# Optimization experiments

Hardware: AMD Instinct MI355X
Metric: run time of the kernel (lower is better)

The kernel has to match this reference:

```python
import jax, jax.numpy as jnp
import numpy as np

N, C_TOTAL, C, H, W = 8, 448, 100, 56, 56


def setup_inputs() -> dict:
    key = jax.random.key(0)
    k1, k2, k3, k4 = jax.random.split(key, 4)
    fmaps = jax.random.normal(k1, (N, C_TOTAL, H, W), dtype=jnp.float32)
    select_index = jax.random.randint(k2, (C,), 0, C_TOTAL)
    mean = jax.random.normal(k3, (C, H, W), dtype=jnp.float32)
    # Per-pixel inverse covariance must be PSD so the quadratic form is >= 0
    A = jax.random.normal(k4, (C, C, H, W), dtype=jnp.float32)
    cov = jnp.einsum('cehw,dehw->cdhw', A, A) / jnp.float32(C)  # (C,C,H,W), PSD per pixel
    return {
        'fmaps': fmaps,
        'select_index': select_index,
        'mean': mean,
        'cov': cov,
        'min_score': jnp.float32(0.0),
        'max_score': jnp.float32(50.0),
    }


def reference(fmaps, select_index, mean, cov, min_score, max_score):
    # x_ = fmaps[:, select_index, ...] - mean  -> (N, C, H, W)
    x = fmaps[:, select_index, :, :] - mean[None]
    # left = sum_c x[n,c,h,w] * cov[c,d,h,w]  (per-pixel matvec), avoids (N,C,C,H,W) intermediate
    left = jnp.einsum('nchw,cdhw->ndhw', x, cov)
    # per-pixel Mahalanobis distance
    s_map = jnp.sqrt(jnp.sum(x * left, axis=1))  # (N, H, W)
    # bilinear upsample x4 (torch Upsample align_corners=False == half-pixel linear resize)
    score_map = jax.image.resize(s_map, (s_map.shape[0], 4 * H, 4 * W), method='linear')
    scores = (score_map - min_score) / (max_score - min_score)
    return jnp.squeeze(scores)
```

## Files before the change

kernel.cpp:

```cpp
#include <hip/hip_runtime.h>
#include <math.h>

#define NN 8
#define C_TOTAL 448
#define CC 100
#define HH 56
#define WW 56
#define HW (HH*WW)
#define NPIX4 (HW/4)
#define OH 224
#define OW 224
#define NT4 13
#define NG 25

typedef __attribute__((ext_vector_type(4))) _Float16 half4;
typedef __attribute__((ext_vector_type(8))) _Float16 half8;
typedef __attribute__((ext_vector_type(4))) float    f32x4;

__device__ __forceinline__ f32x4 cvtlo(const half8 h) {
    return __builtin_convertvector(__builtin_shufflevector(h, h, 0, 1, 2, 3), f32x4);
}
__device__ __forceinline__ f32x4 cvthi(const half8 h) {
    return __builtin_convertvector(__builtin_shufflevector(h, h, 4, 5, 6, 7), f32x4);
}
__device__ __forceinline__ f32x4 fmav(const f32x4 a, const f32x4 b, const f32x4 c) {
    f32x4 r;
    r.x = fmaf(a.x, b.x, c.x);
    r.y = fmaf(a.y, b.y, c.y);
    r.z = fmaf(a.z, b.z, c.z);
    r.w = fmaf(a.w, b.w, c.w);
    return r;
}

__global__ __launch_bounds__(256) void prep_x_kernel(
    const float* __restrict__ fmaps, const int* __restrict__ sel,
    const float* __restrict__ mean, half4* __restrict__ xbuf,
    float* __restrict__ smap)
{
    const int idx = blockIdx.x * 256 + threadIdx.x;
    if (idx < NN * NPIX4) {
        ((float4*)smap)[idx] = make_float4(0.f, 0.f, 0.f, 0.f);
    }
    if (idx >= CC * NPIX4) return;
    const int quad = idx % NPIX4;
    const int c    = idx / NPIX4;

    const float4* f4 = (const float4*)fmaps;
    const float4  m  = ((const float4*)mean)[(size_t)c * NPIX4 + quad];
    const int     sc = sel[c];

    half4 hv[NN];
#pragma unroll
    for (int n = 0; n < NN; ++n) {
        const float4 f = f4[((size_t)n * C_TOTAL + sc) * NPIX4 + quad];
        half4 h;
        h.x = (_Float16)(f.x - m.x);
        h.y = (_Float16)(f.y - m.y);
        h.z = (_Float16)(f.z - m.z);
        h.w = (_Float16)(f.w - m.w);
        hv[n] = h;
    }
    half4* dst = xbuf + ((size_t)c * NPIX4 + quad) * NN;
#pragma unroll
    for (int n = 0; n < NN; ++n) dst[n] = hv[n];
}

__global__ __launch_bounds__(512, 3) void qform_kernel(
    const half4* __restrict__ xbuf, const float* __restrict__ cov,
    float* __restrict__ smap)
{
    __shared__ f32x4 lred[8 * 4 * 64];

    const int tile = blockIdx.x % NT4;
    const int k    = blockIdx.x / NT4;
    const int a    = 4 * k;

    const int w    = threadIdx.x >> 6;
    const int dph  = w & 3;
    const int imgh = w >> 2;
    const int lane = threadIdx.x & 63;
    const int qraw = tile * 64 + lane;
    const bool valid = qraw < NPIX4;
    const int quad = valid ? qraw : (NPIX4 - 1);

    const f32x4* c4 = (const f32x4*)cov;

    f32x4 acc[4][4];
#pragma unroll
    for (int i = 0; i < 4; ++i)
#pragma unroll
        for (int j = 0; j < 4; ++j) acc[i][j] = (f32x4){0.f, 0.f, 0.f, 0.f};

    {
        const int d0 = a + dph;
        const half8* xp = (const half8*)(xbuf + ((size_t)d0 * NPIX4 + quad) * NN + imgh * 4);
        const half8 hA = xp[0];
        const half8 hB = xp[1];
        f32x4 xv[4];
        xv[0] = cvtlo(hA); xv[1] = cvthi(hA);
        xv[2] = cvtlo(hB); xv[3] = cvthi(hB);
#pragma unroll
        for (int i = 0; i < 4; ++i) {
            if (i <= dph) {
                f32x4 cv = __builtin_nontemporal_load(
                    &c4[((size_t)(a + i) * CC + d0) * NPIX4 + quad]);
                if (i == dph) cv *= 0.5f;
#pragma unroll
                for (int j = 0; j < 4; ++j) acc[i][j] = fmav(xv[j], cv, acc[i][j]);
            }
        }
    }

    for (int d = a + 4 + dph; d < CC; d += 4) {
        const half8* xp = (const half8*)(xbuf + ((size_t)d * NPIX4 + quad) * NN + imgh * 4);
        const half8 hA = xp[0];
        const half8 hB = xp[1];
        f32x4 xv[4];
        xv[0] = cvtlo(hA); xv[1] = cvthi(hA);
        xv[2] = cvtlo(hB); xv[3] = cvthi(hB);

        const size_t base = ((size_t)a * CC + d) * NPIX4 + quad;
#pragma unroll
        for (int i = 0; i < 4; ++i) {
            const f32x4 cv = __builtin_nontemporal_load(&c4[base + (size_t)i * CC * NPIX4]);
#pragma unroll
            for (int j = 0; j < 4; ++j) acc[i][j] = fmav(xv[j], cv, acc[i][j]);
        }
    }

    {
        f32x4 part[4];
#pragma unroll
        for (int j = 0; j < 4; ++j) part[j] = (f32x4){0.f, 0.f, 0.f, 0.f};
#pragma unroll
        for (int i = 0; i < 4; ++i) {
            const half8* xp = (const half8*)(xbuf + ((size_t)(a + i) * NPIX4 + quad) * NN + imgh * 4);
            const half8 hA = xp[0];
            const half8 hB = xp[1];
            part[0] = fmav(cvtlo(hA), acc[i][0], part[0]);
            part[1] = fmav(cvthi(hA), acc[i][1], part[1]);
            part[2] = fmav(cvtlo(hB), acc[i][2], part[2]);
            part[3] = fmav(cvthi(hB), acc[i][3], part[3]);
        }
#pragma unroll
        for (int j = 0; j < 4; ++j) {
            part[j] = part[j] + part[j];
            lred[(w * 4 + j) * 64 + lane] = part[j];
        }
    }
    __syncthreads();

    {
        const int im = w;
        const int ih = im >> 2;
        const int sl = im & 3;
        f32x4 s = (f32x4){0.f, 0.f, 0.f, 0.f};
#pragma unroll
        for (int dp = 0; dp < 4; ++dp) {
            s = s + lred[((ih * 4 + dp) * 4 + sl) * 64 + lane];
        }
        if (valid) {
            float* dst = smap + (size_t)im * HW + (size_t)qraw * 4;
            atomicAdd(dst + 0, s.x);
            atomicAdd(dst + 1, s.y);
            atomicAdd(dst + 2, s.z);
            atomicAdd(dst + 3, s.w);
        }
    }
}

__global__ __launch_bounds__(256) void upsample_kernel(
    const float* __restrict__ smap,
    const float* __restrict__ minp, const float* __restrict__ maxp,
    float* __restrict__ out)
{
    const int idx = blockIdx.x * 256 + threadIdx.x;
    const int total = NN * OH * OW;
    if (idx >= total) return;

    const int ox = idx % OW;
    const int oy = (idx / OW) % OH;
    const int n  = idx / (OW * OH);

    const float fy = oy * 0.25f - 0.375f;
    const float fx = ox * 0.25f - 0.375f;

    int y0 = (int)floorf(fy);
    int x0 = (int)floorf(fx);
    const float wy = fy - (float)y0;
    const float wx = fx - (float)x0;
    int y1 = min(y0 + 1, HH - 1); y0 = max(y0, 0);
    int x1 = min(x0 + 1, WW - 1); x0 = max(x0, 0);

    const float* s = smap + (size_t)n * HW;
    const float v00 = sqrtf(fmaxf(s[y0 * WW + x0], 0.f));
    const float v01 = sqrtf(fmaxf(s[y0 * WW + x1], 0.f));
    const float v10 = sqrtf(fmaxf(s[y1 * WW + x0], 0.f));
    const float v11 = sqrtf(fmaxf(s[y1 * WW + x1], 0.f));

    const float v = (1.0f - wy) * ((1.0f - wx) * v00 + wx * v01)
                  +          wy * ((1.0f - wx) * v10 + wx * v11);

    const float mn = *minp;
    const float mx = *maxp;
    out[idx] = (v - mn) / (mx - mn);
}

extern "C" void kernel_launch(void* const* d_in, const int* in_sizes, int n_in,
                              void* d_out, int out_size, void* d_ws, size_t ws_size,
                              hipStream_t stream)
{
    const float* fmaps = (const float*)d_in[0];
    const int*   sel   = (const int*)  d_in[1];
    const float* mean  = (const float*)d_in[2];
    const float* cov   = (const float*)d_in[3];
    const float* minp  = (const float*)d_in[4];
    const float* maxp  = (const float*)d_in[5];
    float* out = (float*)d_out;

    half4* xbuf = (half4*)d_ws;
    float* smap = (float*)((char*)d_ws + (size_t)CC*NPIX4*NN*8);

    {
        const int total = CC * NPIX4;
        prep_x_kernel<<<(total + 255) / 256, 256, 0, stream>>>(fmaps, sel, mean, xbuf, smap);
    }
    qform_kernel<<<NG * NT4, 512, 0, stream>>>(xbuf, cov, smap);
    {
        const int total = NN * OH * OW;
        upsample_kernel<<<(total + 255) / 256, 256, 0, stream>>>(smap, minp, maxp, out);
    }
}
```

Baseline: 221.8 us.

## Split long triangular row groups across two blocks and rebalance warp work

The quadratic-form kernel previously gave each block one 4-row group of the upper triangle, so the early groups carried far more columns than the late ones and the grid was small and unbalanced. Now the first twelve row groups are split at their column midpoint into two blocks each, growing the grid from 325 to 481 blocks. Within a block each warp now owns two rows and handles alternate columns, with the column loop unrolled by two, and the occupancy hint rises to 4 blocks per CU. This is meant to even out per-block work and improve latency hiding, at the cost of more atomics and more repeated x loads.

```diff
diff --git a/kernel.cpp b/kernel.cpp
--- a/kernel.cpp
+++ b/kernel.cpp
@@ -12,6 +12,8 @@
 #define OW 224
 #define NT4 13
 #define NG 25
+#define KSPLIT 12
+#define NKIND (2*KSPLIT + (NG - KSPLIT))
 
 typedef __attribute__((ext_vector_type(4))) _Float16 half4;
 typedef __attribute__((ext_vector_type(8))) _Float16 half8;
@@ -65,83 +67,136 @@
     for (int n = 0; n < NN; ++n) dst[n] = hv[n];
 }
 
-__global__ __launch_bounds__(512, 3) void qform_kernel(
+__global__ __launch_bounds__(512, 4) void qform_kernel(
     const half4* __restrict__ xbuf, const float* __restrict__ cov,
     float* __restrict__ smap)
 {
     __shared__ f32x4 lred[8 * 4 * 64];
 
     const int tile = blockIdx.x % NT4;
-    const int k    = blockIdx.x / NT4;
-    const int a    = 4 * k;
+    const int kind = blockIdx.x / NT4;
+    int k, h, split;
+    if (kind < 2 * KSPLIT) { k = kind >> 1; h = kind & 1; split = 1; }
+    else                   { k = kind - KSPLIT; h = 0; split = 0; }
+    const int a   = 4 * k;
+    const int L   = CC - a;
+    const int mid = a + ((L + 1) >> 1);
 
     const int w    = threadIdx.x >> 6;
-    const int dph  = w & 3;
+    const int dph  = w & 1;
+    const int rh   = (w >> 1) & 1;
     const int imgh = w >> 2;
     const int lane = threadIdx.x & 63;
     const int qraw = tile * 64 + lane;
     const bool valid = qraw < NPIX4;
     const int quad = valid ? qraw : (NPIX4 - 1);
 
-    const f32x4* c4 = (const f32x4*)cov;
-
-    f32x4 acc[4][4];
-#pragma unroll
-    for (int i = 0; i < 4; ++i)
+    const int r0 = a + 2 * rh;
+    const int r1 = r0 + 1;
+
+    const f32x4* c4  = (const f32x4*)cov;
+    const half8* xb8 = (const half8*)xbuf;
+
+    f32x4 acc[2][4];
+#pragma unroll
+    for (int i = 0; i < 2; ++i)
 #pragma unroll
         for (int j = 0; j < 4; ++j) acc[i][j] = (f32x4){0.f, 0.f, 0.f, 0.f};
 
-    {
-        const int d0 = a + dph;
-        const half8* xp = (const half8*)(xbuf + ((size_t)d0 * NPIX4 + quad) * NN + imgh * 4);
+    int lo, hi;
+    if (split && h == 1) {
+        lo = mid + (((mid ^ (a + dph)) & 1));
+        hi = CC;
+    } else {
+        hi = split ? mid : CC;
+        const int d0 = r0 + dph;
+        {
+            const half8* xp = xb8 + ((size_t)d0 * NPIX4 + quad) * 4 + imgh * 2;
+            const half8 hA = xp[0];
+            const half8 hB = xp[1];
+            f32x4 xv[4];
+            xv[0] = cvtlo(hA); xv[1] = cvthi(hA);
+            xv[2] = cvtlo(hB); xv[3] = cvthi(hB);
+            f32x4 cv0 = __builtin_nontemporal_load(&c4[((size_t)r0 * CC + d0) * NPIX4 + quad]);
+            if (dph == 0) {
+                cv0 *= 0.5f;
+#pragma unroll
+                for (int j = 0; j < 4; ++j) acc[0][j] = fmav(xv[j], cv0, acc[0][j]);
+            } else {
+#pragma unroll
+                for (int j = 0; j < 4; ++j) acc[0][j] = fmav(xv[j], cv0, acc[0][j]);
+                f32x4 cv1 = __builtin_nontemporal_load(&c4[((size_t)r1 * CC + d0) * NPIX4 + quad]);
+                cv1 *= 0.5f;
+#pragma unroll
+                for (int j = 0; j < 4; ++j) acc[1][j] = fmav(xv[j], cv1, acc[1][j]);
+            }
+        }
+        lo = r0 + dph + 2;
+    }
+
+    int d = lo;
+    for (; d + 2 < hi; d += 4) {
+        const half8* xp0 = xb8 + ((size_t)d * NPIX4 + quad) * 4 + imgh * 2;
+        const half8* xp1 = xb8 + ((size_t)(d + 2) * NPIX4 + quad) * 4 + imgh * 2;
+        const half8 a0 = xp0[0];
+        const half8 b0 = xp0[1];
+        const half8 a1 = xp1[0];
+        const half8 b1 = xp1[1];
+        const size_t cb0 = ((size_t)r0 * CC + d) * NPIX4 + quad;
+        const size_t cb1 = ((size_t)r1 * CC + d) * NPIX4 + quad;
+        const f32x4 c00 = __builtin_nontemporal_load(&c4[cb0]);
+        const f32x4 c10 = __builtin_nontemporal_load(&c4[cb1]);
+        const f32x4 c01 = __builtin_nontemporal_load(&c4[cb0 + 2 * NPIX4]);
+        const f32x4 c11 = __builtin_nontemporal_load(&c4[cb1 + 2 * NPIX4]);
+
+        {
+            f32x4 xv[4];
+            xv[0] = cvtlo(a0); xv[1] = cvthi(a0);
+            xv[2] = cvtlo(b0); xv[3] = cvthi(b0);
+#pragma unroll
+            for (int j = 0; j < 4; ++j) acc[0][j] = fmav(xv[j], c00, acc[0][j]);
+#pragma unroll
+            for (int j = 0; j < 4; ++j) acc[1][j] = fmav(xv[j], c10, acc[1][j]);
+        }
+        {
+            f32x4 xv[4];
+            xv[0] = cvtlo(a1); xv[1] = cvthi(a1);
+            xv[2] = cvtlo(b1); xv[3] = cvthi(b1);
+#pragma unroll
+            for (int j = 0; j < 4; ++j) acc[0][j] = fmav(xv[j], c01, acc[0][j]);
+#pragma unroll
+            for (int j = 0; j < 4; ++j) acc[1][j] = fmav(xv[j], c11, acc[1][j]);
+        }
+    }
+    if (d < hi) {
+        const half8* xp = xb8 + ((size_t)d * NPIX4 + quad) * 4 + imgh * 2;
         const half8 hA = xp[0];
         const half8 hB = xp[1];
+        const f32x4 c0 = __builtin_nontemporal_load(&c4[((size_t)r0 * CC + d) * NPIX4 + quad]);
+        const f32x4 c1 = __builtin_nontemporal_load(&c4[((size_t)r1 * CC + d) * NPIX4 + quad]);
         f32x4 xv[4];
         xv[0] = cvtlo(hA); xv[1] = cvthi(hA);
         xv[2] = cvtlo(hB); xv[3] = cvthi(hB);
 #pragma unroll
-        for (int i = 0; i < 4; ++i) {
-            if (i <= dph) {
-                f32x4 cv = __builtin_nontemporal_load(
-                    &c4[((size_t)(a + i) * CC + d0) * NPIX4 + quad]);
-                if (i == dph) cv *= 0.5f;
-#pragma unroll
-                for (int j = 0; j < 4; ++j) acc[i][j] = fmav(xv[j], cv, acc[i][j]);
-            }
-        }
-    }
-
-    for (int d = a + 4 + dph; d < CC; d += 4) {
-        const half8* xp = (const half8*)(xbuf + ((size_t)d * NPIX4 + quad) * NN + imgh * 4);
-        const half8 hA = xp[0];
-        const half8 hB = xp[1];
-        f32x4 xv[4];
-        xv[0] = cvtlo(hA); xv[1] = cvthi(hA);
-        xv[2] = cvtlo(hB); xv[3] = cvthi(hB);
-
-        const size_t base = ((size_t)a * CC + d) * NPIX4 + quad;
-#pragma unroll
-        for (int i = 0; i < 4; ++i) {
-            const f32x4 cv = __builtin_nontemporal_load(&c4[base + (size_t)i * CC * NPIX4]);
-#pragma unroll
-            for (int j = 0; j < 4; ++j) acc[i][j] = fmav(xv[j], cv, acc[i][j]);
-        }
-    }
-
-    {
+        for (int j = 0; j < 4; ++j) acc[0][j] = fmav(xv[j], c0, acc[0][j]);
+#pragma unroll
+        for (int j = 0; j < 4; ++j) acc[1][j] = fmav(xv[j], c1, acc[1][j]);
+    }
+
+    {
+        const half8* x0p = xb8 + ((size_t)r0 * NPIX4 + quad) * 4 + imgh * 2;
+        const half8* x1p = xb8 + ((size_t)r1 * NPIX4 + quad) * 4 + imgh * 2;
+        const half8 xa0 = x0p[0], xb0 = x0p[1];
+        const half8 xa1 = x1p[0], xb1 = x1p[1];
         f32x4 part[4];
-#pragma unroll
-        for (int j = 0; j < 4; ++j) part[j] = (f32x4){0.f, 0.f, 0.f, 0.f};
-#pragma unroll
-        for (int i = 0; i < 4; ++i) {
-            const half8* xp = (const half8*)(xbuf + ((size_t)(a + i) * NPIX4 + quad) * NN + imgh * 4);
-            const half8 hA = xp[0];
-            const half8 hB = xp[1];
-            part[0] = fmav(cvtlo(hA), acc[i][0], part[0]);
-            part[1] = fmav(cvthi(hA), acc[i][1], part[1]);
-            part[2] = fmav(cvtlo(hB), acc[i][2], part[2]);
-            part[3] = fmav(cvthi(hB), acc[i][3], part[3]);
-        }
+        part[0] = cvtlo(xa0) * acc[0][0];
+        part[1] = cvthi(xa0) * acc[0][1];
+        part[2] = cvtlo(xb0) * acc[0][2];
+        part[3] = cvthi(xb0) * acc[0][3];
+        part[0] = fmav(cvtlo(xa1), acc[1][0], part[0]);
+        part[1] = fmav(cvthi(xa1), acc[1][1], part[1]);
+        part[2] = fmav(cvtlo(xb1), acc[1][2], part[2]);
+        part[3] = fmav(cvthi(xb1), acc[1][3], part[3]);
 #pragma unroll
         for (int j = 0; j < 4; ++j) {
             part[j] = part[j] + part[j];
@@ -152,12 +207,12 @@
 
     {
         const int im = w;
-        const int ih = im >> 2;
+        const int sh = (im >> 2) * 4;
         const int sl = im & 3;
         f32x4 s = (f32x4){0.f, 0.f, 0.f, 0.f};
 #pragma unroll
-        for (int dp = 0; dp < 4; ++dp) {
-            s = s + lred[((ih * 4 + dp) * 4 + sl) * 64 + lane];
+        for (int sw = 0; sw < 4; ++sw) {
+            s = s + lred[((sh + sw) * 4 + sl) * 64 + lane];
         }
         if (valid) {
             float* dst = smap + (size_t)im * HW + (size_t)qraw * 4;
@@ -225,7 +280,7 @@
         const int total = CC * NPIX4;
         prep_x_kernel<<<(total + 255) / 256, 256, 0, stream>>>(fmaps, sel, mean, xbuf, smap);
     }
-    qform_kernel<<<NG * NT4, 512, 0, stream>>>(xbuf, cov, smap);
+    qform_kernel<<<NKIND * NT4, 512, 0, stream>>>(xbuf, cov, smap);
     {
         const int total = NN * OH * OW;
         upsample_kernel<<<(total + 255) / 256, 256, 0, stream>>>(smap, minp, maxp, out);
```

Measured after the change: 219.2 us. No clear change (-1.2%).

## Stage cov tiles into LDS with async global_load_lds double buffering

Applied to the files above, without the earlier changes.

The qform kernel now streams covariance rows into shared memory in chunks of 8 d-values using global_load_lds, double-buffered so the next chunk loads while the current one is consumed. Work across waves is re-split: each wave owns two of the four rows and alternates d parity, which halves the accumulator registers. Occupancy is raised from 3 to 4 blocks per CU. The cost is extra block-wide barriers per chunk and LDS traffic, and padded tail iterations are masked with zero weights.

```diff
diff --git a/kernel.cpp b/kernel.cpp
--- a/kernel.cpp
+++ b/kernel.cpp
@@ -12,6 +12,7 @@
 #define OW 224
 #define NT4 13
 #define NG 25
+#define CHB 8
 
 typedef __attribute__((ext_vector_type(4))) _Float16 half4;
 typedef __attribute__((ext_vector_type(8))) _Float16 half8;
@@ -31,6 +32,10 @@
     r.w = fmaf(a.w, b.w, c.w);
     return r;
 }
+
+#define GL_LDS(gp, lp) \
+  __builtin_amdgcn_global_load_lds((const __attribute__((address_space(1))) void*)(gp), \
+                                   (__attribute__((address_space(3))) void*)(lp), 16, 0, 0)
 
 __global__ __launch_bounds__(256) void prep_x_kernel(
     const float* __restrict__ fmaps, const int* __restrict__ sel,
@@ -65,83 +70,130 @@
     for (int n = 0; n < NN; ++n) dst[n] = hv[n];
 }
 
-__global__ __launch_bounds__(512, 3) void qform_kernel(
+__global__ __launch_bounds__(512, 4) void qform_kernel(
     const half4* __restrict__ xbuf, const float* __restrict__ cov,
     float* __restrict__ smap)
 {
-    __shared__ f32x4 lred[8 * 4 * 64];
+    __shared__ __align__(16) char ldsraw[2 * CHB * 4 * 64 * 16];
 
     const int tile = blockIdx.x % NT4;
     const int k    = blockIdx.x / NT4;
     const int a    = 4 * k;
 
     const int w    = threadIdx.x >> 6;
-    const int dph  = w & 3;
+    const int cph  = w & 1;
+    const int rh   = (w >> 1) & 1;
     const int imgh = w >> 2;
     const int lane = threadIdx.x & 63;
     const int qraw = tile * 64 + lane;
     const bool valid = qraw < NPIX4;
     const int quad = valid ? qraw : (NPIX4 - 1);
 
-    const f32x4* c4 = (const f32x4*)cov;
-
-    f32x4 acc[4][4];
-#pragma unroll
-    for (int i = 0; i < 4; ++i)
+    const int r0 = a + 2 * rh;
+    const int r1 = r0 + 1;
+
+    const half8* xb8 = (const half8*)xbuf;
+    f32x4* covlds = (f32x4*)ldsraw;
+
+    const int S0  = a + 4;
+    const int nch = (CC - S0 + CHB - 1) / CHB;
+
+    f32x4 acc[2][4];
+#pragma unroll
+    for (int i = 0; i < 2; ++i)
 #pragma unroll
         for (int j = 0; j < 4; ++j) acc[i][j] = (f32x4){0.f, 0.f, 0.f, 0.f};
 
-    {
-        const int d0 = a + dph;
-        const half8* xp = (const half8*)(xbuf + ((size_t)d0 * NPIX4 + quad) * NN + imgh * 4);
+    if (nch > 0) {
+        const int d  = S0 + w;
+        const int dc = (d < CC) ? d : (CC - 1);
+#pragma unroll
+        for (int i = 0; i < 4; ++i) {
+            const float* g = cov + ((size_t)(a + i) * CC + dc) * HW + (size_t)quad * 4;
+            GL_LDS(g, (char*)&covlds[((0 * CHB + w) * 4 + i) * 64]);
+        }
+    }
+
+#pragma unroll
+    for (int dd = 0; dd < 2; ++dd) {
+        const int d = a + 2 * dd + cph;
+        const half8* xp = xb8 + ((size_t)d * NPIX4 + quad) * 4 + imgh * 2;
         const half8 hA = xp[0];
         const half8 hB = xp[1];
         f32x4 xv[4];
         xv[0] = cvtlo(hA); xv[1] = cvthi(hA);
         xv[2] = cvtlo(hB); xv[3] = cvthi(hB);
 #pragma unroll
-        for (int i = 0; i < 4; ++i) {
-            if (i <= dph) {
+        for (int i = 0; i < 2; ++i) {
+            const int r = r0 + i;
+            if (r <= d) {
                 f32x4 cv = __builtin_nontemporal_load(
-                    &c4[((size_t)(a + i) * CC + d0) * NPIX4 + quad]);
-                if (i == dph) cv *= 0.5f;
+                    (const f32x4*)(cov + ((size_t)r * CC + d) * HW + (size_t)quad * 4));
+                if (r == d) cv *= 0.5f;
 #pragma unroll
                 for (int j = 0; j < 4; ++j) acc[i][j] = fmav(xv[j], cv, acc[i][j]);
             }
         }
     }
 
-    for (int d = a + 4 + dph; d < CC; d += 4) {
-        const half8* xp = (const half8*)(xbuf + ((size_t)d * NPIX4 + quad) * NN + imgh * 4);
-        const half8 hA = xp[0];
-        const half8 hB = xp[1];
-        f32x4 xv[4];
-        xv[0] = cvtlo(hA); xv[1] = cvthi(hA);
-        xv[2] = cvtlo(hB); xv[3] = cvthi(hB);
-
-        const size_t base = ((size_t)a * CC + d) * NPIX4 + quad;
-#pragma unroll
-        for (int i = 0; i < 4; ++i) {
-            const f32x4 cv = __builtin_nontemporal_load(&c4[base + (size_t)i * CC * NPIX4]);
-#pragma unroll
-            for (int j = 0; j < 4; ++j) acc[i][j] = fmav(xv[j], cv, acc[i][j]);
-        }
-    }
-
-    {
+    if (nch > 0) {
+        asm volatile("s_waitcnt vmcnt(0)" ::: "memory");
+        __syncthreads();
+        int buf = 0;
+        for (int ch = 0; ch < nch; ++ch) {
+            if (ch + 1 < nch) {
+                const int d  = S0 + (ch + 1) * CHB + w;
+                const int dc = (d < CC) ? d : (CC - 1);
+#pragma unroll
+                for (int i = 0; i < 4; ++i) {
+                    const float* g = cov + ((size_t)(a + i) * CC + dc) * HW + (size_t)quad * 4;
+                    GL_LDS(g, (char*)&covlds[(((buf ^ 1) * CHB + w) * 4 + i) * 64]);
+                }
+            }
+            const int cb = S0 + ch * CHB;
+#pragma unroll
+            for (int ci = 0; ci < 4; ++ci) {
+                const int cl = 2 * ci + cph;
+                const int d  = cb + cl;
+                const float wt = (d < CC) ? 1.f : 0.f;
+                const int  dc  = (d < CC) ? d : (CC - 1);
+                const half8* xp = xb8 + ((size_t)dc * NPIX4 + quad) * 4 + imgh * 2;
+                const half8 hA = xp[0];
+                const half8 hB = xp[1];
+                f32x4 xv[4];
+                xv[0] = cvtlo(hA); xv[1] = cvthi(hA);
+                xv[2] = cvtlo(hB); xv[3] = cvthi(hB);
+                f32x4 cv0 = covlds[((buf * CHB + cl) * 4 + 2 * rh + 0) * 64 + lane];
+                f32x4 cv1 = covlds[((buf * CHB + cl) * 4 + 2 * rh + 1) * 64 + lane];
+                cv0 *= wt;
+                cv1 *= wt;
+#pragma unroll
+                for (int j = 0; j < 4; ++j) acc[0][j] = fmav(xv[j], cv0, acc[0][j]);
+#pragma unroll
+                for (int j = 0; j < 4; ++j) acc[1][j] = fmav(xv[j], cv1, acc[1][j]);
+            }
+            asm volatile("s_waitcnt vmcnt(0)" ::: "memory");
+            __syncthreads();
+            buf ^= 1;
+        }
+    }
+
+    __syncthreads();
+    f32x4* lred = (f32x4*)ldsraw;
+    {
+        const half8* x0p = xb8 + ((size_t)r0 * NPIX4 + quad) * 4 + imgh * 2;
+        const half8* x1p = xb8 + ((size_t)r1 * NPIX4 + quad) * 4 + imgh * 2;
+        const half8 xa0 = x0p[0], xb0 = x0p[1];
+        const half8 xa1 = x1p[0], xb1 = x1p[1];
         f32x4 part[4];
-#pragma unroll
-        for (int j = 0; j < 4; ++j) part[j] = (f32x4){0.f, 0.f, 0.f, 0.f};
-#pragma unroll
-        for (int i = 0; i < 4; ++i) {
-            const half8* xp = (const half8*)(xbuf + ((size_t)(a + i) * NPIX4 + quad) * NN + imgh * 4);
-            const half8 hA = xp[0];
-            const half8 hB = xp[1];
-            part[0] = fmav(cvtlo(hA), acc[i][0], part[0]);
-            part[1] = fmav(cvthi(hA), acc[i][1], part[1]);
-            part[2] = fmav(cvtlo(hB), acc[i][2], part[2]);
-            part[3] = fmav(cvthi(hB), acc[i][3], part[3]);
-        }
+        part[0] = cvtlo(xa0) * acc[0][0];
+        part[1] = cvthi(xa0) * acc[0][1];
+        part[2] = cvtlo(xb0) * acc[0][2];
+        part[3] = cvthi(xb0) * acc[0][3];
+        part[0] = fmav(cvtlo(xa1), acc[1][0], part[0]);
+        part[1] = fmav(cvthi(xa1), acc[1][1], part[1]);
+        part[2] = fmav(cvtlo(xb1), acc[1][2], part[2]);
+        part[3] = fmav(cvthi(xb1), acc[1][3], part[3]);
 #pragma unroll
         for (int j = 0; j < 4; ++j) {
             part[j] = part[j] + part[j];
@@ -152,12 +204,12 @@
 
     {
         const int im = w;
-        const int ih = im >> 2;
+        const int sh = (im >> 2) * 4;
         const int sl = im & 3;
         f32x4 s = (f32x4){0.f, 0.f, 0.f, 0.f};
 #pragma unroll
-        for (int dp = 0; dp < 4; ++dp) {
-            s = s + lred[((ih * 4 + dp) * 4 + sl) * 64 + lane];
+        for (int sw = 0; sw < 4; ++sw) {
+            s = s + lred[((sh + sw) * 4 + sl) * 64 + lane];
         }
         if (valid) {
             float* dst = smap + (size_t)im * HW + (size_t)qraw * 4;
```

Result: no change. 224.8 us (+1.4%).
